# Kernel tuning notes

Measured on AMD Instinct MI355X. Metric: run time of the kernel, lower is better.

The kernel has to match this reference:

```python
import jax, jax.numpy as jnp
import numpy as np

E = 128          # number of bot groups (envs)
NB = 256         # bots per group
DQ = DK = DV = 256
D = DQ + DK + DV # 768
COM_RANGE = 15.0
KV_NOISE = 0.05
NEG = -1000000.0


def setup_inputs() -> dict:
    key = jax.random.key(0)
    k1, k2, k3, k4 = jax.random.split(key, 4)
    N = E * NB
    qkv = jax.random.normal(k1, (N, D), dtype=jnp.float32)
    # audibility mask: [N_total, n_per_group]; mask[bot_slice] -> [n, n] per group
    mask = jax.random.bernoulli(k2, 0.9, (N, NB))
    # 2D positions in a 30x30 arena so ~half of pairs fall within com_range
    bot_pos = jax.random.uniform(k3, (N, 2), dtype=jnp.float32, minval=0.0, maxval=30.0)
    # kv noise: zero on the q part [:K_DIM], gaussian(std=kv_noise) on k,v part
    noise = jnp.concatenate(
        [jnp.zeros((N, DQ), jnp.float32),
         KV_NOISE * jax.random.normal(k4, (N, DK + DV), dtype=jnp.float32)],
        axis=-1)
    s = jnp.float32(0.0)  # nn.Parameter init
    return {"qkv": qkv, "mask": mask, "bot_pos": bot_pos, "noise": noise, "s": s}


def reference(qkv, mask, bot_pos, noise, s):
    # noise injection on k,v channels (noise is zero on q channels)
    qkv = qkv + noise
    scale_s = jnp.abs(s) + 1.0

    # all bot groups are equal-sized -> batch the per-slice loop as [E, NB, ...]
    qkv_g = qkv.reshape(E, NB, D)
    q = qkv_g[..., :DQ] * scale_s
    k = qkv_g[..., DQ:DQ + DK]
    v = qkv_g[..., DQ + DK:]

    # pairwise-distance range mask per group
    pos = bot_pos.reshape(E, NB, 2)
    bdiff = pos[:, None, :, :] - pos[:, :, None, :]          # [E, NB, NB, 2]
    range_mask = jnp.linalg.norm(bdiff, axis=-1) < COM_RANGE  # [E, NB, NB]

    audible = mask.reshape(E, NB, NB) & range_mask            # [E, NB, NB]

    # SDPA with additive mask (torch adds -1e6 where masked)
    scores = jnp.einsum('eqd,ekd->eqk', q, k) / jnp.sqrt(jnp.float32(DK))
    scores = scores + jnp.where(audible, 0.0, NEG)
    attn = jax.nn.softmax(scores, axis=-1)
    x = jnp.einsum('eqk,ekd->eqd', attn, v)                   # [E, NB, DV]

    # zero out bots that hear nobody
    x = x * audible.any(axis=-1, keepdims=True)
    return x.reshape(E * NB, DV)
```

## Files before the change

### kernel.cpp

```cpp
#include <hip/hip_runtime.h>
#include <hip/hip_bf16.h>
#include <stdint.h>


#define EE   128
#define NBB  256
#define DDIM 768
#define NEGV (-1000000.0f)

typedef __attribute__((ext_vector_type(8))) short short8;
typedef __attribute__((ext_vector_type(4))) float f32x4;

__device__ __forceinline__ unsigned short f2bf(float f){
  union { float f; unsigned u; } v; v.f = f;
  return (unsigned short)((v.u + 0x7FFFu + ((v.u >> 16) & 1u)) >> 16);
}
__device__ __forceinline__ unsigned short cvt1(float f){
  __hip_bfloat16 h = __float2bfloat16(f);
  unsigned short u; __builtin_memcpy(&u, &h, 2); return u;
}
__device__ __forceinline__ unsigned pk2(float lo, float hi){
  return (unsigned)cvt1(lo) | ((unsigned)cvt1(hi) << 16);
}

__device__ __forceinline__ void swap32(unsigned &a, unsigned &b){
#if __has_builtin(__builtin_amdgcn_permlane32_swap)
  auto r = __builtin_amdgcn_permlane32_swap(a, b, false, false);
  a = r[0]; b = r[1];
#else
  const int up = threadIdx.x & 32;
  const unsigned ax = __shfl_xor(a, 32), bx = __shfl_xor(b, 32);
  const unsigned na = up ? bx : a, nb = up ? b : ax;
  a = na; b = nb;
#endif
}
__device__ __forceinline__ void swap16(unsigned &a, unsigned &b){
#if __has_builtin(__builtin_amdgcn_permlane16_swap)
  auto r = __builtin_amdgcn_permlane16_swap(a, b, false, false);
  a = r[0]; b = r[1];
#else
  const int odd = threadIdx.x & 16;
  const unsigned ax = __shfl_xor(a, 16), bx = __shfl_xor(b, 16);
  const unsigned na = odd ? bx : a, nb = odd ? b : ax;
  a = na; b = nb;
#endif
}

__device__ __forceinline__ void gload16(const void* g, void* l){
  __builtin_amdgcn_global_load_lds((const __attribute__((address_space(1))) unsigned*)g,
                                   (__attribute__((address_space(3))) unsigned*)l, 16, 0, 0);
}
__device__ __forceinline__ void gstage(const unsigned short* __restrict__ base,
                                       unsigned short* __restrict__ buf,
                                       int wave, int lane){
  #pragma unroll
  for(int i = 0; i < 8; ++i){
    const int lrow = wave*16 + i*2 + (lane >> 5);
    const int col  = ((lane & 31) * 8) ^ ((lrow & 7) << 3);
    gload16(base + (size_t)lrow * 256 + col, buf + (wave*16 + i*2) * 256);
  }
}

__global__ void k_prep(const float* __restrict__ qkv, const float* __restrict__ noise,
                       unsigned short* __restrict__ Vt, unsigned short* __restrict__ Kb){
  __shared__ unsigned short tile[64 * 66];
  if(blockIdx.x < 2048){
    const int b = blockIdx.x;
    const int e = b >> 4, t4 = b & 15;
    const int k0 = (t4 >> 2) << 6, d0 = (t4 & 3) << 6;
    const int u = threadIdx.x & 15, r = threadIdx.x >> 4;
    #pragma unroll
    for(int i = 0; i < 4; ++i){
      const int kl = r + (i << 4);
      const size_t off = ((size_t)(e*NBB + k0 + kl)) * DDIM + 512 + d0 + (u << 2);
      f32x4 v  = *(const f32x4*)(qkv   + off);
      f32x4 nz = *(const f32x4*)(noise + off);
      const int base = kl * 66 + (u << 2);
      tile[base+0] = f2bf(v[0]+nz[0]); tile[base+1] = f2bf(v[1]+nz[1]);
      tile[base+2] = f2bf(v[2]+nz[2]); tile[base+3] = f2bf(v[3]+nz[3]);
    }
    __syncthreads();
    #pragma unroll
    for(int i = 0; i < 4; ++i){
      const int dl = r + (i << 4);
      unsigned short o0 = tile[(u*4+0)*66 + dl];
      unsigned short o1 = tile[(u*4+1)*66 + dl];
      unsigned short o2 = tile[(u*4+2)*66 + dl];
      unsigned short o3 = tile[(u*4+3)*66 + dl];
      *(ushort4*)(Vt + ((size_t)(e*NBB + d0 + dl)) * NBB + k0 + (u << 2)) =
          make_ushort4(o0, o1, o2, o3);
    }
  } else {
    const int b2 = blockIdx.x - 2048;
    const int n  = b2*8 + (threadIdx.x >> 5);
    const int col = (threadIdx.x & 31) * 8;
    const size_t off = (size_t)n * DDIM + 256 + col;
    f32x4 a0 = *(const f32x4*)(qkv + off),   a1 = *(const f32x4*)(qkv + off + 4);
    f32x4 n0 = *(const f32x4*)(noise + off), n1 = *(const f32x4*)(noise + off + 4);
    short8 o;
    o[0]=f2bf(a0[0]+n0[0]); o[1]=f2bf(a0[1]+n0[1]); o[2]=f2bf(a0[2]+n0[2]); o[3]=f2bf(a0[3]+n0[3]);
    o[4]=f2bf(a1[0]+n1[0]); o[5]=f2bf(a1[1]+n1[1]); o[6]=f2bf(a1[2]+n1[2]); o[7]=f2bf(a1[3]+n1[3]);
    *(short8*)(Kb + (size_t)n * 256 + col) = o;
  }
}

__launch_bounds__(256, 2)
__global__ void k_attn(const float* __restrict__ qkv, const float* __restrict__ sp,
                       const unsigned char* __restrict__ m8, const int* __restrict__ m32,
                       const float* __restrict__ pos,
                       const unsigned short* __restrict__ Vt,
                       const unsigned short* __restrict__ Kb,
                       float* __restrict__ out){
  extern __shared__ unsigned char smem[];
  unsigned short* buf0 = (unsigned short*)smem;
  unsigned short* buf1 = (unsigned short*)(smem + 32768);
  unsigned*       audL = (unsigned*)(smem + 65536);
  float*          posx = (float*)(smem + 67584);
  float*          posy = (float*)(smem + 68608);

  const int bid = blockIdx.x;
  const int e   = ((bid & 7) << 4) + (bid >> 5);
  const int qq  = (bid >> 3) & 3;
  const int tid  = threadIdx.x;
  const int wave = tid >> 6;
  const int lane = tid & 63;
  const int g    = lane >> 4;
  const int u    = lane & 15;
  const int q0   = qq * 64 + wave * 16;
  const size_t ebase = (size_t)e * NBB;

  {
    const float2 p = *(const float2*)(pos + (ebase + tid) * 2);
    posx[tid] = p.x; posy[tid] = p.y;
  }
  const unsigned probe = ((const unsigned*)m32)[tid & 63];
  const int isInt = !__any(probe > 1u);
  __syncthreads();

  gstage(Kb + ebase * 256, buf0, wave, lane);

  #pragma unroll
  for(int h = 0; h < 2; ++h){
    const int w   = tid + h * 256;
    const int row = w >> 3;
    const int j   = w & 7;
    const float qx = posx[qq*64 + row], qy = posy[qq*64 + row];
    const size_t mbase = (ebase + qq*64 + row) * NBB + j * 32;
    unsigned wd = 0u;
    if(isInt){
      #pragma unroll
      for(int ii = 0; ii < 8; ++ii){
        const int blk = (ii + j) & 7;
        const int4 mv = *(const int4*)(m32 + mbase + blk * 4);
        const int mvals[4] = {mv.x, mv.y, mv.z, mv.w};
        #pragma unroll
        for(int jj = 0; jj < 4; ++jj){
          const int kk = blk * 4 + jj;
          const int k  = j * 32 + kk;
          const float dx = posx[k] - qx, dy = posy[k] - qy;
          const float d2 = __fadd_rn(__fmul_rn(dx, dx), __fmul_rn(dy, dy));
          if((mvals[jj] != 0) && (sqrtf(d2) < 15.0f)) wd |= 1u << kk;
        }
      }
    } else {
      #pragma unroll
      for(int i = 0; i < 2; ++i){
        const int4 mv = *(const int4*)(m8 + mbase + i * 16);
        const int mvals[4] = {mv.x, mv.y, mv.z, mv.w};
        #pragma unroll
        for(int jt = 0; jt < 4; ++jt){
          const int jj = (jt + j) & 3;
          #pragma unroll
          for(int b = 0; b < 4; ++b){
            const int kk = i * 16 + jj * 4 + b;
            const int k  = j * 32 + kk;
            const float dx = posx[k] - qx, dy = posy[k] - qy;
            const float d2 = __fadd_rn(__fmul_rn(dx, dx), __fmul_rn(dy, dy));
            if((((unsigned)mvals[jj] >> (8 * b)) & 0xFFu) && (sqrtf(d2) < 15.0f)) wd |= 1u << kk;
          }
        }
      }
    }
    audL[w] = wd;
  }

  const float scale = fabsf(sp[0]) + 1.0f;
  short8 qf[8];
  {
    const float* qrow = qkv + (ebase + q0 + u) * DDIM;
    #pragma unroll
    for(int dk = 0; dk < 8; ++dk){
      f32x4 a = *(const f32x4*)(qrow + dk*32 + g*8);
      f32x4 b = *(const f32x4*)(qrow + dk*32 + g*8 + 4);
      short8 f;
      f[0]=cvt1(a[0]*scale); f[1]=cvt1(a[1]*scale); f[2]=cvt1(a[2]*scale); f[3]=cvt1(a[3]*scale);
      f[4]=cvt1(b[0]*scale); f[5]=cvt1(b[1]*scale); f[6]=cvt1(b[2]*scale); f[7]=cvt1(b[3]*scale);
      qf[dk] = f;
    }
  }

  const f32x4 zero4 = {0.f, 0.f, 0.f, 0.f};
  f32x4 acc[16];
  #pragma unroll
  for(int nt = 0; nt < 16; ++nt) acc[nt] = zero4;

  __syncthreads();

  #pragma unroll
  for(int kq = 0; kq < 4; ++kq){
    unsigned short* cur = (kq & 1) ? buf1 : buf0;
    unsigned short* nxt = (kq & 1) ? buf0 : buf1;
    if(kq < 3) gstage(Kb + (ebase + (size_t)(kq+1) * 64) * 256, nxt, wave, lane);
    else       gstage(Vt + ebase * 256, nxt, wave, lane);
    #pragma unroll
    for(int nth = 0; nth < 4; ++nth){
      const unsigned short* kr = cur + (nth*16 + u) * 256;
      const int sw = (u & 7) << 3;
      #pragma unroll
      for(int dk = 0; dk < 8; ++dk){
        short8 kb = *(const short8*)(kr + ((dk*32 + g*8) ^ sw));
        acc[kq*4 + nth] = __builtin_amdgcn_mfma_f32_16x16x32_bf16(kb, qf[dk], acc[kq*4 + nth], 0, 0, 0);
      }
    }
    if(kq < 3) __syncthreads();
  }

  unsigned wmask[8];
  {
    const unsigned* arow = audL + (wave*16 + u) * 8;
    #pragma unroll
    for(int j = 0; j < 8; ++j) wmask[j] = arow[j];
  }
  const unsigned anyw = wmask[0]|wmask[1]|wmask[2]|wmask[3]|wmask[4]|wmask[5]|wmask[6]|wmask[7];
  const unsigned long long rowsAny = __ballot(anyw != 0u);

  float m0=-3.0e38f, m1=-3.0e38f, m2=-3.0e38f, m3=-3.0e38f;
  #pragma unroll
  for(int nt = 0; nt < 16; ++nt){
    const unsigned wv = wmask[nt >> 1] >> (((nt & 1) << 4) + g*4);
    f32x4 s = acc[nt];
    s[0] = s[0]*0.0625f + ((wv      & 1u) ? 0.0f : NEGV);
    s[1] = s[1]*0.0625f + (((wv>>1) & 1u) ? 0.0f : NEGV);
    s[2] = s[2]*0.0625f + (((wv>>2) & 1u) ? 0.0f : NEGV);
    s[3] = s[3]*0.0625f + (((wv>>3) & 1u) ? 0.0f : NEGV);
    acc[nt] = s;
    m0 = fmaxf(m0, s[0]); m1 = fmaxf(m1, s[1]);
    m2 = fmaxf(m2, s[2]); m3 = fmaxf(m3, s[3]);
  }
  float mx = fmaxf(fmaxf(m0, m1), fmaxf(m2, m3));
  mx = fmaxf(mx, __shfl_xor(mx, 16));
  mx = fmaxf(mx, __shfl_xor(mx, 32));
  float s0=0.f, s1=0.f, s2=0.f, s3=0.f;
  #pragma unroll
  for(int nt = 0; nt < 16; ++nt){
    f32x4 p = acc[nt];
    p[0] = __expf(p[0] - mx); p[1] = __expf(p[1] - mx);
    p[2] = __expf(p[2] - mx); p[3] = __expf(p[3] - mx);
    acc[nt] = p;
    s0 += p[0]; s1 += p[1]; s2 += p[2]; s3 += p[3];
  }
  float ssum = (s0 + s1) + (s2 + s3);
  ssum += __shfl_xor(ssum, 16);
  ssum += __shfl_xor(ssum, 32);
  const float inv = 1.0f / ssum;

  short8 pa[8];
  #pragma unroll
  for(int kt = 0; kt < 8; ++kt){
    unsigned cE = pk2(acc[2*kt][0]*inv,   acc[2*kt][1]*inv);
    unsigned dE = pk2(acc[2*kt][2]*inv,   acc[2*kt][3]*inv);
    unsigned cO = pk2(acc[2*kt+1][0]*inv, acc[2*kt+1][1]*inv);
    unsigned dO = pk2(acc[2*kt+1][2]*inv, acc[2*kt+1][3]*inv);
    swap32(cE, cO); swap16(cE, cO);
    swap32(dE, dO); swap16(dE, dO);
    union { short8 s; unsigned w[4]; } pk;
    pk.w[0] = cE; pk.w[1] = dE; pk.w[2] = cO; pk.w[3] = dO;
    pa[kt] = pk.s;
  }

  __syncthreads();

  #pragma unroll
  for(int dqt = 0; dqt < 4; ++dqt){
    unsigned short* cur = (dqt & 1) ? buf1 : buf0;
    unsigned short* nxt = (dqt & 1) ? buf0 : buf1;
    if(dqt < 3) gstage(Vt + (ebase + (size_t)(dqt+1) * 64) * 256, nxt, wave, lane);
    f32x4 xacc[4];
    #pragma unroll
    for(int dt = 0; dt < 4; ++dt) xacc[dt] = zero4;
    #pragma unroll
    for(int dt = 0; dt < 4; ++dt){
      const unsigned short* vr = cur + (dt*16 + u) * 256;
      const int sw = (u & 7) << 3;
      #pragma unroll
      for(int kt = 0; kt < 8; ++kt){
        short8 bv = *(const short8*)(vr + ((kt*32 + g*8) ^ sw));
        xacc[dt] = __builtin_amdgcn_mfma_f32_16x16x32_bf16(pa[kt], bv, xacc[dt], 0, 0, 0);
      }
    }
    #pragma unroll
    for(int r = 0; r < 4; ++r){
      const float zf = ((rowsAny >> (g*4 + r)) & 1ull) ? 1.0f : 0.0f;
      float* orow = out + (ebase + q0 + g*4 + r) * 256 + dqt*64;
      #pragma unroll
      for(int dt = 0; dt < 4; ++dt)
        orow[dt*16 + u] = xacc[dt][r] * zf;
    }
    if(dqt < 3) __syncthreads();
  }
}

extern "C" void kernel_launch(void* const* d_in, const int* in_sizes, int n_in,
                              void* d_out, int out_size, void* d_ws, size_t ws_size,
                              hipStream_t stream){
  (void)in_sizes; (void)n_in; (void)out_size; (void)ws_size;
  const float* qkv   = (const float*)d_in[0];
  const void*  mask  = d_in[1];
  const float* pos   = (const float*)d_in[2];
  const float* noise = (const float*)d_in[3];
  const float* sp    = (const float*)d_in[4];

  unsigned short* Vt = (unsigned short*)d_ws;
  unsigned short* Kb = (unsigned short*)((unsigned char*)d_ws + 16777216);
  float* outp = (float*)d_out;

  k_prep<<<6144, 256, 0, stream>>>(qkv, noise, Vt, Kb);

  hipFuncSetAttribute((const void*)k_attn, hipFuncAttributeMaxDynamicSharedMemorySize, 69632);
  k_attn<<<512, 256, 69632, stream>>>(qkv, sp,
                                      (const unsigned char*)mask, (const int*)mask,
                                      pos, Vt, Kb, outp);
}
```

Measured before the change: 65.78 us.

## Merge K conversion and V transpose into one 64-row block per prep CTA

The prep kernel is restructured so each of 512 blocks handles 64 rows of one group, converting both the K slice and the full 256-wide V slice (transposed via a larger 33KB LDS tile). This replaces the previous 6144 small blocks split between V-transpose and K-convert roles. Fewer, fatter blocks cut launch/scheduling overhead and give per-thread contiguous loads, at the cost of per-thread strided 64-float row accesses (threads read 256B-separated chunks, worse coalescing) and lower parallelism and occupancy from the big shared tile.

New measurement: 78.32 us. 19.1% more time.

```diff
diff --git a/kernel.cpp b/kernel.cpp
--- a/kernel.cpp
+++ b/kernel.cpp
@@ -63,44 +63,59 @@
 
 __global__ void k_prep(const float* __restrict__ qkv, const float* __restrict__ noise,
                        unsigned short* __restrict__ Vt, unsigned short* __restrict__ Kb){
-  __shared__ unsigned short tile[64 * 66];
-  if(blockIdx.x < 2048){
-    const int b = blockIdx.x;
-    const int e = b >> 4, t4 = b & 15;
-    const int k0 = (t4 >> 2) << 6, d0 = (t4 & 3) << 6;
-    const int u = threadIdx.x & 15, r = threadIdx.x >> 4;
-    #pragma unroll
-    for(int i = 0; i < 4; ++i){
-      const int kl = r + (i << 4);
-      const size_t off = ((size_t)(e*NBB + k0 + kl)) * DDIM + 512 + d0 + (u << 2);
-      f32x4 v  = *(const f32x4*)(qkv   + off);
-      f32x4 nz = *(const f32x4*)(noise + off);
-      const int base = kl * 66 + (u << 2);
-      tile[base+0] = f2bf(v[0]+nz[0]); tile[base+1] = f2bf(v[1]+nz[1]);
-      tile[base+2] = f2bf(v[2]+nz[2]); tile[base+3] = f2bf(v[3]+nz[3]);
-    }
-    __syncthreads();
-    #pragma unroll
-    for(int i = 0; i < 4; ++i){
-      const int dl = r + (i << 4);
-      unsigned short o0 = tile[(u*4+0)*66 + dl];
-      unsigned short o1 = tile[(u*4+1)*66 + dl];
-      unsigned short o2 = tile[(u*4+2)*66 + dl];
-      unsigned short o3 = tile[(u*4+3)*66 + dl];
-      *(ushort4*)(Vt + ((size_t)(e*NBB + d0 + dl)) * NBB + k0 + (u << 2)) =
-          make_ushort4(o0, o1, o2, o3);
-    }
-  } else {
-    const int b2 = blockIdx.x - 2048;
-    const int n  = b2*8 + (threadIdx.x >> 5);
-    const int col = (threadIdx.x & 31) * 8;
-    const size_t off = (size_t)n * DDIM + 256 + col;
-    f32x4 a0 = *(const f32x4*)(qkv + off),   a1 = *(const f32x4*)(qkv + off + 4);
-    f32x4 n0 = *(const f32x4*)(noise + off), n1 = *(const f32x4*)(noise + off + 4);
-    short8 o;
-    o[0]=f2bf(a0[0]+n0[0]); o[1]=f2bf(a0[1]+n0[1]); o[2]=f2bf(a0[2]+n0[2]); o[3]=f2bf(a0[3]+n0[3]);
-    o[4]=f2bf(a1[0]+n1[0]); o[5]=f2bf(a1[1]+n1[1]); o[6]=f2bf(a1[2]+n1[2]); o[7]=f2bf(a1[3]+n1[3]);
-    *(short8*)(Kb + (size_t)n * 256 + col) = o;
+  __shared__ unsigned short tile[4 * 64 * 66];
+  const int b  = blockIdx.x;
+  const int e  = b >> 2;
+  const int k0 = (b & 3) << 6;
+  const int tid = threadIdx.x;
+  const int t8  = tid & 7;
+
+  #pragma unroll
+  for(int pass = 0; pass < 2; ++pass){
+    const int row = (tid >> 3) + pass * 32;
+    const int n   = e * NBB + k0 + row;
+    const size_t goff = (size_t)n * DDIM + 256 + t8 * 64;
+    if(t8 < 4){
+      #pragma unroll
+      for(int c = 0; c < 8; ++c){
+        f32x4 a0 = *(const f32x4*)(qkv + goff + c*8);
+        f32x4 a1 = *(const f32x4*)(qkv + goff + c*8 + 4);
+        f32x4 z0 = *(const f32x4*)(noise + goff + c*8);
+        f32x4 z1 = *(const f32x4*)(noise + goff + c*8 + 4);
+        short8 o;
+        o[0]=f2bf(a0[0]+z0[0]); o[1]=f2bf(a0[1]+z0[1]); o[2]=f2bf(a0[2]+z0[2]); o[3]=f2bf(a0[3]+z0[3]);
+        o[4]=f2bf(a1[0]+z1[0]); o[5]=f2bf(a1[1]+z1[1]); o[6]=f2bf(a1[2]+z1[2]); o[7]=f2bf(a1[3]+z1[3]);
+        *(short8*)(Kb + (size_t)n * 256 + t8*64 + c*8) = o;
+      }
+    } else {
+      const int s = t8 - 4;
+      unsigned short* trow = tile + (s*64 + row) * 66;
+      #pragma unroll
+      for(int c = 0; c < 16; ++c){
+        f32x4 a = *(const f32x4*)(qkv + goff + c*4);
+        f32x4 z = *(const f32x4*)(noise + goff + c*4);
+        unsigned lo = pk2(a[0]+z[0], a[1]+z[1]);
+        unsigned hi = pk2(a[2]+z[2], a[3]+z[3]);
+        *(unsigned*)(trow + c*4)     = lo;
+        *(unsigned*)(trow + c*4 + 2) = hi;
+      }
+    }
+  }
+  __syncthreads();
+
+  const int s  = tid >> 6;
+  const int u  = tid & 15;
+  const int r4 = (tid >> 4) & 3;
+  const unsigned short* tbase = tile + s * 64 * 66;
+  #pragma unroll
+  for(int i = 0; i < 16; ++i){
+    const int dl = r4 * 16 + i;
+    unsigned short o0 = tbase[(u*4+0)*66 + dl];
+    unsigned short o1 = tbase[(u*4+1)*66 + dl];
+    unsigned short o2 = tbase[(u*4+2)*66 + dl];
+    unsigned short o3 = tbase[(u*4+3)*66 + dl];
+    *(ushort4*)(Vt + ((size_t)(e*NBB + s*64 + dl)) * NBB + k0 + u*4) =
+        make_ushort4(o0, o1, o2, o3);
   }
 }
 
@@ -324,7 +339,7 @@
   unsigned short* Kb = (unsigned short*)((unsigned char*)d_ws + 16777216);
   float* outp = (float*)d_out;
 
-  k_prep<<<6144, 256, 0, stream>>>(qkv, noise, Vt, Kb);
+  k_prep<<<512, 256, 0, stream>>>(qkv, noise, Vt, Kb);
 
   hipFuncSetAttribute((const void*)k_attn, hipFuncAttributeMaxDynamicSharedMemorySize, 69632);
   k_attn<<<512, 256, 69632, stream>>>(qkv, sp,
```

## Load K and V fragments directly from global instead of LDS double-buffering

Applied to the files above, without the earlier changes.

Removes the LDS staging path for K and V tiles (global_load_lds with swizzle and double buffers). Each wave now reads its bf16 K and V MFMA operands straight from global memory, relying on L2/L1 for the reuse across the four waves of a block. The Q fragment load is also hoisted above the mask computation so its latency overlaps that work. Block-wide syncs and about 64KB of dynamic LDS are dropped, which could raise occupancy, but each wave now issues redundant global loads for the same K/V rows and the fragment loads are strided. A no-op +0.0f is also added to the distance computation in the byte-mask path.

After: 113.5 us. +72.5%, slower.

```diff
diff --git a/kernel.cpp b/kernel.cpp
--- a/kernel.cpp
+++ b/kernel.cpp
@@ -44,21 +44,6 @@
   const unsigned na = odd ? bx : a, nb = odd ? b : ax;
   a = na; b = nb;
 #endif
-}
-
-__device__ __forceinline__ void gload16(const void* g, void* l){
-  __builtin_amdgcn_global_load_lds((const __attribute__((address_space(1))) unsigned*)g,
-                                   (__attribute__((address_space(3))) unsigned*)l, 16, 0, 0);
-}
-__device__ __forceinline__ void gstage(const unsigned short* __restrict__ base,
-                                       unsigned short* __restrict__ buf,
-                                       int wave, int lane){
-  #pragma unroll
-  for(int i = 0; i < 8; ++i){
-    const int lrow = wave*16 + i*2 + (lane >> 5);
-    const int col  = ((lane & 31) * 8) ^ ((lrow & 7) << 3);
-    gload16(base + (size_t)lrow * 256 + col, buf + (wave*16 + i*2) * 256);
-  }
 }
 
 __global__ void k_prep(const float* __restrict__ qkv, const float* __restrict__ noise,
@@ -111,12 +96,8 @@
                        const unsigned short* __restrict__ Vt,
                        const unsigned short* __restrict__ Kb,
                        float* __restrict__ out){
-  extern __shared__ unsigned char smem[];
-  unsigned short* buf0 = (unsigned short*)smem;
-  unsigned short* buf1 = (unsigned short*)(smem + 32768);
-  unsigned*       audL = (unsigned*)(smem + 65536);
-  float*          posx = (float*)(smem + 67584);
-  float*          posy = (float*)(smem + 68608);
+  __shared__ unsigned audL[512];
+  __shared__ float posx[NBB], posy[NBB];
 
   const int bid = blockIdx.x;
   const int e   = ((bid & 7) << 4) + (bid >> 5);
@@ -137,7 +118,20 @@
   const int isInt = !__any(probe > 1u);
   __syncthreads();
 
-  gstage(Kb + ebase * 256, buf0, wave, lane);
+  const float scale = fabsf(sp[0]) + 1.0f;
+  short8 qf[8];
+  {
+    const float* qrow = qkv + (ebase + q0 + u) * DDIM;
+    #pragma unroll
+    for(int dk = 0; dk < 8; ++dk){
+      f32x4 a = *(const f32x4*)(qrow + dk*32 + g*8);
+      f32x4 b = *(const f32x4*)(qrow + dk*32 + g*8 + 4);
+      short8 f;
+      f[0]=cvt1(a[0]*scale); f[1]=cvt1(a[1]*scale); f[2]=cvt1(a[2]*scale); f[3]=cvt1(a[3]*scale);
+      f[4]=cvt1(b[0]*scale); f[5]=cvt1(b[1]*scale); f[6]=cvt1(b[2]*scale); f[7]=cvt1(b[3]*scale);
+      qf[dk] = f;
+    }
+  }
 
   #pragma unroll
   for(int h = 0; h < 2; ++h){
@@ -175,7 +169,7 @@
             const int kk = i * 16 + jj * 4 + b;
             const int k  = j * 32 + kk;
             const float dx = posx[k] - qx, dy = posy[k] - qy;
-            const float d2 = __fadd_rn(__fmul_rn(dx, dx), __fmul_rn(dy, dy));
+            const float d2 = __fadd_rn(__fmul_rn(dx, dx), __fadd_rn(__fmul_rn(dy, dy), 0.0f));
             if((((unsigned)mvals[jj] >> (8 * b)) & 0xFFu) && (sqrtf(d2) < 15.0f)) wd |= 1u << kk;
           }
         }
@@ -184,46 +178,25 @@
     audL[w] = wd;
   }
 
-  const float scale = fabsf(sp[0]) + 1.0f;
-  short8 qf[8];
-  {
-    const float* qrow = qkv + (ebase + q0 + u) * DDIM;
-    #pragma unroll
-    for(int dk = 0; dk < 8; ++dk){
-      f32x4 a = *(const f32x4*)(qrow + dk*32 + g*8);
-      f32x4 b = *(const f32x4*)(qrow + dk*32 + g*8 + 4);
-      short8 f;
-      f[0]=cvt1(a[0]*scale); f[1]=cvt1(a[1]*scale); f[2]=cvt1(a[2]*scale); f[3]=cvt1(a[3]*scale);
-      f[4]=cvt1(b[0]*scale); f[5]=cvt1(b[1]*scale); f[6]=cvt1(b[2]*scale); f[7]=cvt1(b[3]*scale);
-      qf[dk] = f;
-    }
-  }
-
   const f32x4 zero4 = {0.f, 0.f, 0.f, 0.f};
   f32x4 acc[16];
   #pragma unroll
   for(int nt = 0; nt < 16; ++nt) acc[nt] = zero4;
 
+  {
+    const unsigned short* kbase = Kb + (ebase + u) * 256 + g*8;
+    #pragma unroll
+    for(int t = 0; t < 16; ++t){
+      const unsigned short* kr = kbase + t * 16 * 256;
+      #pragma unroll
+      for(int dk = 0; dk < 8; ++dk){
+        short8 kb = *(const short8*)(kr + dk*32);
+        acc[t] = __builtin_amdgcn_mfma_f32_16x16x32_bf16(kb, qf[dk], acc[t], 0, 0, 0);
+      }
+    }
+  }
+
   __syncthreads();
-
-  #pragma unroll
-  for(int kq = 0; kq < 4; ++kq){
-    unsigned short* cur = (kq & 1) ? buf1 : buf0;
-    unsigned short* nxt = (kq & 1) ? buf0 : buf1;
-    if(kq < 3) gstage(Kb + (ebase + (size_t)(kq+1) * 64) * 256, nxt, wave, lane);
-    else       gstage(Vt + ebase * 256, nxt, wave, lane);
-    #pragma unroll
-    for(int nth = 0; nth < 4; ++nth){
-      const unsigned short* kr = cur + (nth*16 + u) * 256;
-      const int sw = (u & 7) << 3;
-      #pragma unroll
-      for(int dk = 0; dk < 8; ++dk){
-        short8 kb = *(const short8*)(kr + ((dk*32 + g*8) ^ sw));
-        acc[kq*4 + nth] = __builtin_amdgcn_mfma_f32_16x16x32_bf16(kb, qf[dk], acc[kq*4 + nth], 0, 0, 0);
-      }
-    }
-    if(kq < 3) __syncthreads();
-  }
 
   unsigned wmask[8];
   {
@@ -278,23 +251,17 @@
     pa[kt] = pk.s;
   }
 
-  __syncthreads();
-
   #pragma unroll
   for(int dqt = 0; dqt < 4; ++dqt){
-    unsigned short* cur = (dqt & 1) ? buf1 : buf0;
-    unsigned short* nxt = (dqt & 1) ? buf0 : buf1;
-    if(dqt < 3) gstage(Vt + (ebase + (size_t)(dqt+1) * 64) * 256, nxt, wave, lane);
     f32x4 xacc[4];
     #pragma unroll
     for(int dt = 0; dt < 4; ++dt) xacc[dt] = zero4;
     #pragma unroll
     for(int dt = 0; dt < 4; ++dt){
-      const unsigned short* vr = cur + (dt*16 + u) * 256;
-      const int sw = (u & 7) << 3;
+      const unsigned short* vr = Vt + (ebase + dqt*64 + dt*16 + u) * 256 + g*8;
       #pragma unroll
       for(int kt = 0; kt < 8; ++kt){
-        short8 bv = *(const short8*)(vr + ((kt*32 + g*8) ^ sw));
+        short8 bv = *(const short8*)(vr + kt*32);
         xacc[dt] = __builtin_amdgcn_mfma_f32_16x16x32_bf16(pa[kt], bv, xacc[dt], 0, 0, 0);
       }
     }
@@ -306,7 +273,6 @@
       for(int dt = 0; dt < 4; ++dt)
         orow[dt*16 + u] = xacc[dt][r] * zf;
     }
-    if(dqt < 3) __syncthreads();
   }
 }
 
@@ -325,9 +291,7 @@
   float* outp = (float*)d_out;
 
   k_prep<<<6144, 256, 0, stream>>>(qkv, noise, Vt, Kb);
-
-  hipFuncSetAttribute((const void*)k_attn, hipFuncAttributeMaxDynamicSharedMemorySize, 69632);
-  k_attn<<<512, 256, 69632, stream>>>(qkv, sp,
-                                      (const unsigned char*)mask, (const int*)mask,
-                                      pos, Vt, Kb, outp);
-}
+  k_attn<<<512, 256, 0, stream>>>(qkv, sp,
+                                  (const unsigned char*)mask, (const int*)mask,
+                                  pos, Vt, Kb, outp);
+}
```
